# Optimization experiments

Measured on AMD Instinct MI355X. Metric: run time of the kernel, lower is better.

Reference implementation:

```python
import jax, jax.numpy as jnp
import numpy as np

VOCAB, EMBED = 100000, 128
B, QLEN, DLEN = 1024, 32, 256
KERNEL_NUM, SIGMA, EXACT_SIGMA = 11, 0.1, 0.001
EPS = 1e-8  # torch F.cosine_similarity eps


def _kernel_mus(n):
    l_mu = [1.0]
    if n == 1:
        return l_mu
    bin_size = 2.0 / (n - 1)
    l_mu.append(1 - bin_size / 2)
    for i in range(1, n - 1):
        l_mu.append(round(l_mu[i] - bin_size, 5))
    return list(reversed(l_mu))


def _kernel_sigmas(n, sigma, exact_sigma):
    l_sigma = [exact_sigma]
    if n == 1:
        return l_sigma
    l_sigma += [sigma] * (n - 1)
    return list(reversed(l_sigma))


MUS = jnp.asarray(np.array(_kernel_mus(KERNEL_NUM), dtype=np.float32))      # [K]
SIGMAS = jnp.asarray(np.array(_kernel_sigmas(KERNEL_NUM, SIGMA, EXACT_SIGMA), dtype=np.float32))  # [K]


def setup_inputs() -> dict:
    key = jax.random.key(0)
    k = jax.random.split(key, 7)
    return {
        "emb": jax.random.normal(k[0], (VOCAB, EMBED), dtype=jnp.float32),
        "mlp_w": jax.random.normal(k[1], (1, KERNEL_NUM), dtype=jnp.float32) * 0.3,
        "mlp_b": jax.random.normal(k[2], (1,), dtype=jnp.float32) * 0.1,
        "query1": jax.random.randint(k[3], (B, QLEN), 0, VOCAB, dtype=jnp.int32).astype(jnp.int64),
        "doc1": jax.random.randint(k[4], (B, DLEN), 0, VOCAB, dtype=jnp.int32).astype(jnp.int64),
        "query2": jax.random.randint(k[5], (B, QLEN), 0, VOCAB, dtype=jnp.int32).astype(jnp.int64),
        "doc2": jax.random.randint(k[6], (B, DLEN), 0, VOCAB, dtype=jnp.int32).astype(jnp.int64),
    }


def _predict(emb, mlp_w, mlp_b, query, doc):
    qe = emb[query]                               # [B,Q,E]
    de = emb[doc]                                 # [B,D,E]
    qn = jnp.linalg.norm(qe, axis=-1)             # [B,Q]
    dn = jnp.linalg.norm(de, axis=-1)             # [B,D]
    dots = jnp.einsum("bqe,bde->bqd", qe, de)    # [B,Q,D]
    sim = dots / jnp.maximum(qn[:, :, None] * dn[:, None, :], EPS)
    # multi-Gaussian soft histogram: exp(-(sim-mu)^2/(2 sigma^2)), sum over doc,
    # log1p, sum over query  -> [B,K]
    z = (sim[..., None] - MUS) / SIGMAS           # [B,Q,D,K]
    K = jnp.exp(-0.5 * z * z)
    pooled = jnp.log1p(K.sum(axis=2)).sum(axis=1)  # [B,K]
    return pooled @ mlp_w.T + mlp_b               # [B,1]


def reference(emb, mlp_w, mlp_b, query1, doc1, query2, doc2):
    logits_1 = _predict(emb, mlp_w, mlp_b, query1, doc1)
    logits_2 = _predict(emb, mlp_w, mlp_b, query2, doc2)
    return jax.nn.sigmoid(logits_1 - logits_2)    # [B,1]
```

## Files before the change

kernel.cpp:

```cpp
#include <hip/hip_runtime.h>
#include <math.h>
#include <stdint.h>

#define VOCAB 100000
#define NB    1024
#define QLEN  32
#define DLEN  256
#define EMBED 128
#define KNUM  11

typedef __attribute__((ext_vector_type(8))) short bf16x8;
typedef __attribute__((ext_vector_type(4))) float f32x4;

#define HALF_L2E 0.7213475204444817f
#define TWO_L2E  2.8853900817779268f
#define EM4      0.018315638888734179f

#define SSTR  68
#define SHALF (16 * SSTR)

__device__ __forceinline__ float ex2(float x)
{
    float r;
    asm("v_exp_f32 %0, %1" : "=v"(r) : "v"(x));
    return r;
}

__global__ __launch_bounds__(256)
void cvt_table(const float* __restrict__ emb, ushort* __restrict__ ebf,
               float* __restrict__ inorm)
{
    const int row = blockIdx.x * 8 + (threadIdx.x >> 5);
    const int l32 = threadIdx.x & 31;
    const float4 v = *((const float4*)(emb + (size_t)row * EMBED) + l32);
    union { float f; unsigned u; } x0, x1, x2, x3;
    x0.f = v.x; x1.f = v.y; x2.f = v.z; x3.f = v.w;
    const unsigned r0 = x0.u + 0x8000u, r1 = x1.u + 0x8000u;
    const unsigned r2 = x2.u + 0x8000u, r3 = x3.u + 0x8000u;
    uint2 packed;
    packed.x = (r0 >> 16) | (r1 & 0xFFFF0000u);
    packed.y = (r2 >> 16) | (r3 & 0xFFFF0000u);
    *((uint2*)(ebf + (size_t)row * EMBED) + l32) = packed;
    x0.u = r0 & 0xFFFF0000u; x1.u = r1 & 0xFFFF0000u;
    x2.u = r2 & 0xFFFF0000u; x3.u = r3 & 0xFFFF0000u;
    float n = x0.f * x0.f + x1.f * x1.f + x2.f * x2.f + x3.f * x3.f;
    #pragma unroll
    for (int m = 1; m < 32; m <<= 1) n += __shfl_xor(n, m);
    if (l32 == 0) inorm[row] = __builtin_amdgcn_rsqf(n);
}

__device__ __forceinline__ bf16x8 cvt8(const float* p, float& nacc)
{
    uint4 a = *((const uint4*)p);
    uint4 b = *((const uint4*)(p + 4));
    unsigned u[8] = {a.x, a.y, a.z, a.w, b.x, b.y, b.z, b.w};
    bf16x8 r;
    #pragma unroll
    for (int i = 0; i < 8; ++i) {
        const unsigned q = u[i] + 0x8000u;
        r[i] = (short)(q >> 16);
        union { unsigned uu; float ff; } g; g.uu = q & 0xFFFF0000u;
        nacc = fmaf(g.ff, g.ff, nacc);
    }
    return r;
}

__device__ __forceinline__ void pool_half(float* __restrict__ wtile,
                                          const f32x4* __restrict__ a,
                                          const float* __restrict__ riq,
                                          const float* __restrict__ idn,
                                          float (*__restrict__ stot)[12],
                                          int mtbase, int l15, int quad)
{
    #pragma unroll
    for (int nt = 0; nt < 4; ++nt)
        #pragma unroll
        for (int r = 0; r < 4; ++r)
            wtile[(quad * 4 + r) * SSTR + nt * 16 + l15] = a[nt][r] * riq[r] * idn[nt];

    const float* rp = wtile + l15 * SSTR + quad * 16;
    float ksum[KNUM];
    #pragma unroll
    for (int k = 0; k < KNUM; ++k) ksum[k] = 0.f;

    #pragma unroll
    for (int i = 0; i < 4; ++i) {
        const f32x4 sv = *((const f32x4*)(rp + 4 * i));
        #pragma unroll
        for (int e = 0; e < 4; ++e) {
            const float s  = sv[e];
            const float z  = fmaf(s, 10.f, -1.f);
            const float e0 = ex2(-HALF_L2E * (z * z));
            float ru = ex2(fmaf(z,  TWO_L2E, -TWO_L2E));
            float rd = ex2(fmaf(z, -TWO_L2E, -TWO_L2E));
            ksum[5] += e0;
            float tt = e0;
            tt *= ru; ksum[6] += tt; ru *= EM4;
            tt *= ru; ksum[7] += tt; ru *= EM4;
            tt *= ru; ksum[8] += tt; ru *= EM4;
            tt *= ru; ksum[9] += tt;
            tt = e0;
            tt *= rd; ksum[4] += tt; rd *= EM4;
            tt *= rd; ksum[3] += tt; rd *= EM4;
            tt *= rd; ksum[2] += tt; rd *= EM4;
            tt *= rd; ksum[1] += tt; rd *= EM4;
            tt *= rd; ksum[0] += tt;
            ksum[10] += (s > 0.995f) ? 1.f : 0.f;
        }
    }
    #pragma unroll
    for (int k = 0; k < KNUM; ++k) {
        ksum[k] += __shfl_xor(ksum[k], 16);
        ksum[k] += __shfl_xor(ksum[k], 32);
    }
    if (quad == 0) {
        #pragma unroll
        for (int k = 0; k < KNUM; ++k)
            atomicAdd(&stot[mtbase + l15][k], ksum[k]);
    }
}

__global__ __launch_bounds__(256, 3)
void knrm_pair4(const ushort* __restrict__ ebf,
                const float* __restrict__ inorm,
                const float* __restrict__ mlp_w,
                const int* __restrict__ q1, const int* __restrict__ d1,
                const int* __restrict__ q2, const int* __restrict__ d2,
                float* __restrict__ logits)
{
    const int b    = blockIdx.x;
    const int pair = blockIdx.y;
    const int t    = threadIdx.x;
    const int w    = t >> 6;
    const int l15  = t & 15;
    const int quad = (t & 63) >> 4;

    const int* __restrict__ qry = (pair == 0 ? q1 : q2) + b * QLEN;
    const int* __restrict__ doc = (pair == 0 ? d1 : d2) + b * DLEN;

    __shared__ __align__(16) float s_sim[4 * SHALF];
    __shared__ float s_tot[QLEN][12];

    const int qid0 = qry[l15], qid1 = qry[l15 + 16];
    int did[4];
    #pragma unroll
    for (int j = 0; j < 4; ++j) did[j] = doc[(w * 4 + j) * 16 + l15];

    bf16x8 a0[4], a1[4], bbf[4][4];
    {
        const ushort* qp0 = ebf + (size_t)qid0 * EMBED + quad * 8;
        const ushort* qp1 = ebf + (size_t)qid1 * EMBED + quad * 8;
        #pragma unroll
        for (int kk = 0; kk < 4; ++kk) {
            a0[kk] = *(const bf16x8*)(qp0 + kk * 32);
            a1[kk] = *(const bf16x8*)(qp1 + kk * 32);
        }
        #pragma unroll
        for (int j = 0; j < 4; ++j) {
            const ushort* dp = ebf + (size_t)did[j] * EMBED + quad * 8;
            #pragma unroll
            for (int kk = 0; kk < 4; ++kk)
                bbf[j][kk] = *(const bf16x8*)(dp + kk * 32);
        }
    }
    float idn[4];
    #pragma unroll
    for (int j = 0; j < 4; ++j) idn[j] = inorm[did[j]];
    float riq[2][4];
    #pragma unroll
    for (int r = 0; r < 4; ++r) {
        riq[0][r] = inorm[qry[quad * 4 + r]];
        riq[1][r] = inorm[qry[16 + quad * 4 + r]];
    }

    #pragma unroll
    for (int i = t; i < QLEN * 12; i += 256) ((float*)s_tot)[i] = 0.f;

    #pragma unroll
    for (int kk = 0; kk < 4; ++kk)
        asm volatile("" :: "v"(a0[kk]), "v"(a1[kk]));
    #pragma unroll
    for (int j = 0; j < 4; ++j)
        asm volatile("" :: "v"(bbf[j][0]), "v"(bbf[j][1]),
                          "v"(bbf[j][2]), "v"(bbf[j][3]));
    __builtin_amdgcn_sched_barrier(0);

    f32x4 acc[2][4];
    #pragma unroll
    for (int mt = 0; mt < 2; ++mt)
        #pragma unroll
        for (int j = 0; j < 4; ++j)
            acc[mt][j] = (f32x4){0.f, 0.f, 0.f, 0.f};
    #pragma unroll
    for (int kk = 0; kk < 4; ++kk)
        #pragma unroll
        for (int j = 0; j < 4; ++j) {
            acc[0][j] = __builtin_amdgcn_mfma_f32_16x16x32_bf16(a0[kk], bbf[j][kk], acc[0][j], 0, 0, 0);
            acc[1][j] = __builtin_amdgcn_mfma_f32_16x16x32_bf16(a1[kk], bbf[j][kk], acc[1][j], 0, 0, 0);
        }

    __syncthreads();

    float* wtile = s_sim + w * SHALF;
    pool_half(wtile, acc[0], riq[0], idn, s_tot, 0,  l15, quad);
    pool_half(wtile, acc[1], riq[1], idn, s_tot, 16, l15, quad);
    __syncthreads();

    if (t < QLEN) {
        float c = 0.f;
        #pragma unroll
        for (int k = 0; k < KNUM; ++k) c += mlp_w[k] * log1pf(s_tot[t][k]);
        #pragma unroll
        for (int mm = 1; mm < 32; mm <<= 1) c += __shfl_xor(c, mm);
        if (t == 0) logits[pair * NB + b] = c;
    }
}

template<bool PRE>
__global__ __launch_bounds__(256, 4)
void knrm_pair(const float* __restrict__ emb,
               const ushort* __restrict__ ebf,
               const float* __restrict__ inorm,
               const float* __restrict__ mlp_w,
               const int* __restrict__ q1, const int* __restrict__ d1,
               const int* __restrict__ q2, const int* __restrict__ d2,
               float* __restrict__ logits)
{
    const int b    = blockIdx.x;
    const int pair = blockIdx.y;
    const int t    = threadIdx.x;
    const int w    = t >> 6;
    const int l15  = t & 15;
    const int quad = (t & 63) >> 4;

    const int* __restrict__ qry = (pair == 0 ? q1 : q2) + b * QLEN;
    const int* __restrict__ doc = (pair == 0 ? d1 : d2) + b * DLEN;

    __shared__ __align__(16) float s_sim[4 * SHALF];
    __shared__ float s_tot[QLEN][12];

    #pragma unroll
    for (int i = t; i < QLEN * 12; i += 256) ((float*)s_tot)[i] = 0.f;
    __syncthreads();

    const int qid0 = qry[l15], qid1 = qry[l15 + 16];
    int did[4];
    #pragma unroll
    for (int nt = 0; nt < 4; ++nt) did[nt] = doc[(w * 4 + nt) * 16 + l15];

    f32x4 acc[2][4];
    #pragma unroll
    for (int mt = 0; mt < 2; ++mt)
        #pragma unroll
        for (int nt = 0; nt < 4; ++nt)
            acc[mt][nt] = (f32x4){0.f, 0.f, 0.f, 0.f};

    float idn[4], riq[2][4];
    float* wtile = s_sim + w * SHALF;

    if (PRE) {
        const ushort* qp0 = ebf + (size_t)qid0 * EMBED + quad * 8;
        const ushort* qp1 = ebf + (size_t)qid1 * EMBED + quad * 8;
        #pragma unroll
        for (int kk = 0; kk < 4; ++kk) {
            const bf16x8 a0 = *((const bf16x8*)(qp0 + kk * 32));
            const bf16x8 a1 = *((const bf16x8*)(qp1 + kk * 32));
            #pragma unroll
            for (int nt = 0; nt < 4; ++nt) {
                const bf16x8 bb = *((const bf16x8*)(ebf + (size_t)did[nt] * EMBED + quad * 8 + kk * 32));
                acc[0][nt] = __builtin_amdgcn_mfma_f32_16x16x32_bf16(a0, bb, acc[0][nt], 0, 0, 0);
                acc[1][nt] = __builtin_amdgcn_mfma_f32_16x16x32_bf16(a1, bb, acc[1][nt], 0, 0, 0);
            }
        }
        #pragma unroll
        for (int nt = 0; nt < 4; ++nt) idn[nt] = inorm[did[nt]];
        #pragma unroll
        for (int r = 0; r < 4; ++r) {
            riq[0][r] = inorm[qry[quad * 4 + r]];
            riq[1][r] = inorm[qry[16 + quad * 4 + r]];
        }
    } else {
        float qn2[2] = {0.f, 0.f}, dn2[4] = {0.f, 0.f, 0.f, 0.f};
        const float* qp0 = emb + (size_t)qid0 * EMBED + quad * 8;
        const float* qp1 = emb + (size_t)qid1 * EMBED + quad * 8;
        #pragma unroll
        for (int kk = 0; kk < 4; ++kk) {
            const bf16x8 a0 = cvt8(qp0 + kk * 32, qn2[0]);
            const bf16x8 a1 = cvt8(qp1 + kk * 32, qn2[1]);
            #pragma unroll
            for (int nt = 0; nt < 4; ++nt) {
                const bf16x8 bb = cvt8(emb + (size_t)did[nt] * EMBED + quad * 8 + kk * 32, dn2[nt]);
                acc[0][nt] = __builtin_amdgcn_mfma_f32_16x16x32_bf16(a0, bb, acc[0][nt], 0, 0, 0);
                acc[1][nt] = __builtin_amdgcn_mfma_f32_16x16x32_bf16(a1, bb, acc[1][nt], 0, 0, 0);
            }
        }
        #pragma unroll
        for (int i = 0; i < 2; ++i) {
            qn2[i] += __shfl_xor(qn2[i], 16);
            qn2[i] += __shfl_xor(qn2[i], 32);
        }
        #pragma unroll
        for (int nt = 0; nt < 4; ++nt) {
            dn2[nt] += __shfl_xor(dn2[nt], 16);
            dn2[nt] += __shfl_xor(dn2[nt], 32);
            idn[nt] = __builtin_amdgcn_rsqf(dn2[nt]);
        }
        #pragma unroll
        for (int r = 0; r < 4; ++r) {
            riq[0][r] = __builtin_amdgcn_rsqf(__shfl(qn2[0], quad * 4 + r));
            riq[1][r] = __builtin_amdgcn_rsqf(__shfl(qn2[1], quad * 4 + r));
        }
    }

    pool_half(wtile, acc[0], riq[0], idn, s_tot, 0,  l15, quad);
    pool_half(wtile, acc[1], riq[1], idn, s_tot, 16, l15, quad);
    __syncthreads();

    if (t < QLEN) {
        float c = 0.f;
        #pragma unroll
        for (int k = 0; k < KNUM; ++k) c += mlp_w[k] * log1pf(s_tot[t][k]);
        #pragma unroll
        for (int mm = 1; mm < 32; mm <<= 1) c += __shfl_xor(c, mm);
        if (t == 0) logits[pair * NB + b] = c;
    }
}

__global__ __launch_bounds__(256)
void knrm_combine(const float* __restrict__ logits, float* __restrict__ out)
{
    const int i = blockIdx.x * blockDim.x + threadIdx.x;
    if (i < NB) {
        const float d = logits[i] - logits[NB + i];
        out[i] = 1.f / (1.f + __expf(-d));
    }
}

extern "C" void kernel_launch(void* const* d_in, const int* in_sizes, int n_in,
                              void* d_out, int out_size, void* d_ws, size_t ws_size,
                              hipStream_t stream)
{
    const float* emb   = (const float*)d_in[0];
    const float* mlp_w = (const float*)d_in[1];
    const int* q1 = (const int*)d_in[3];
    const int* d1 = (const int*)d_in[4];
    const int* q2 = (const int*)d_in[5];
    const int* d2 = (const int*)d_in[6];

    float* out = (float*)d_out;

    const size_t need = 2 * NB * 4
                      + (size_t)VOCAB * 4
                      + (size_t)VOCAB * EMBED * 2 + 256;
    if (ws_size >= need) {
        float*  logits = (float*)d_ws;
        float*  inorm  = logits + 2 * NB;
        ushort* ebf    = (ushort*)(inorm + VOCAB);
        cvt_table<<<VOCAB / 8, 256, 0, stream>>>(emb, ebf, inorm);
        knrm_pair4<<<dim3(NB, 2), 256, 0, stream>>>(ebf, inorm, mlp_w,
                                                    q1, d1, q2, d2, logits);
    } else {
        float* logits = (float*)d_ws;
        knrm_pair<false><<<dim3(NB, 2), 256, 0, stream>>>(emb, nullptr, nullptr, mlp_w,
                                                          q1, d1, q2, d2, logits);
    }
    knrm_combine<<<(NB + 255) / 256, 256, 0, stream>>>((float*)d_ws, out);
}
```

Measured before the change: 137.9 us.

## Process both query/doc pairs per block, prefetching pair B during pair A pooling

Each block now handles both pairs for one batch row. Pair B's embedding gathers are issued before pair A's pooling so their latency overlaps with the pooling arithmetic, and the sigmoid combine is folded into the kernel, which drops the separate combine launch. The price is more live registers under a 3-wave occupancy bound and half as many blocks, which could cause spills or lower parallelism. The dead PRE path of the fallback kernel is also removed.

New measurement: 150.9 us. 9.4% more time.

```diff
diff --git a/kernel.cpp b/kernel.cpp
--- a/kernel.cpp
+++ b/kernel.cpp
@@ -121,35 +121,36 @@
 }
 
 __global__ __launch_bounds__(256, 3)
-void knrm_pair4(const ushort* __restrict__ ebf,
-                const float* __restrict__ inorm,
-                const float* __restrict__ mlp_w,
-                const int* __restrict__ q1, const int* __restrict__ d1,
-                const int* __restrict__ q2, const int* __restrict__ d2,
-                float* __restrict__ logits)
+void knrm_pair12(const ushort* __restrict__ ebf,
+                 const float* __restrict__ inorm,
+                 const float* __restrict__ mlp_w,
+                 const int* __restrict__ q1, const int* __restrict__ d1,
+                 const int* __restrict__ q2, const int* __restrict__ d2,
+                 float* __restrict__ out)
 {
     const int b    = blockIdx.x;
-    const int pair = blockIdx.y;
     const int t    = threadIdx.x;
     const int w    = t >> 6;
     const int l15  = t & 15;
     const int quad = (t & 63) >> 4;
 
-    const int* __restrict__ qry = (pair == 0 ? q1 : q2) + b * QLEN;
-    const int* __restrict__ doc = (pair == 0 ? d1 : d2) + b * DLEN;
+    const int* __restrict__ qryA = q1 + b * QLEN;
+    const int* __restrict__ docA = d1 + b * DLEN;
+    const int* __restrict__ qryB = q2 + b * QLEN;
+    const int* __restrict__ docB = d2 + b * DLEN;
 
     __shared__ __align__(16) float s_sim[4 * SHALF];
-    __shared__ float s_tot[QLEN][12];
-
-    const int qid0 = qry[l15], qid1 = qry[l15 + 16];
-    int did[4];
-    #pragma unroll
-    for (int j = 0; j < 4; ++j) did[j] = doc[(w * 4 + j) * 16 + l15];
+    __shared__ float s_tot[2][QLEN][12];
+
+    const int qidA0 = qryA[l15], qidA1 = qryA[l15 + 16];
+    int didA[4];
+    #pragma unroll
+    for (int j = 0; j < 4; ++j) didA[j] = docA[(w * 4 + j) * 16 + l15];
 
     bf16x8 a0[4], a1[4], bbf[4][4];
     {
-        const ushort* qp0 = ebf + (size_t)qid0 * EMBED + quad * 8;
-        const ushort* qp1 = ebf + (size_t)qid1 * EMBED + quad * 8;
+        const ushort* qp0 = ebf + (size_t)qidA0 * EMBED + quad * 8;
+        const ushort* qp1 = ebf + (size_t)qidA1 * EMBED + quad * 8;
         #pragma unroll
         for (int kk = 0; kk < 4; ++kk) {
             a0[kk] = *(const bf16x8*)(qp0 + kk * 32);
@@ -157,24 +158,24 @@
         }
         #pragma unroll
         for (int j = 0; j < 4; ++j) {
-            const ushort* dp = ebf + (size_t)did[j] * EMBED + quad * 8;
+            const ushort* dp = ebf + (size_t)didA[j] * EMBED + quad * 8;
             #pragma unroll
             for (int kk = 0; kk < 4; ++kk)
                 bbf[j][kk] = *(const bf16x8*)(dp + kk * 32);
         }
     }
-    float idn[4];
-    #pragma unroll
-    for (int j = 0; j < 4; ++j) idn[j] = inorm[did[j]];
-    float riq[2][4];
+    float idnA[4];
+    #pragma unroll
+    for (int j = 0; j < 4; ++j) idnA[j] = inorm[didA[j]];
+    float riqA[2][4];
     #pragma unroll
     for (int r = 0; r < 4; ++r) {
-        riq[0][r] = inorm[qry[quad * 4 + r]];
-        riq[1][r] = inorm[qry[16 + quad * 4 + r]];
-    }
-
-    #pragma unroll
-    for (int i = t; i < QLEN * 12; i += 256) ((float*)s_tot)[i] = 0.f;
+        riqA[0][r] = inorm[qryA[quad * 4 + r]];
+        riqA[1][r] = inorm[qryA[16 + quad * 4 + r]];
+    }
+
+    #pragma unroll
+    for (int i = t; i < 2 * QLEN * 12; i += 256) ((float*)s_tot)[i] = 0.f;
 
     #pragma unroll
     for (int kk = 0; kk < 4; ++kk)
@@ -185,34 +186,93 @@
                           "v"(bbf[j][2]), "v"(bbf[j][3]));
     __builtin_amdgcn_sched_barrier(0);
 
-    f32x4 acc[2][4];
+    f32x4 accA[2][4];
     #pragma unroll
     for (int mt = 0; mt < 2; ++mt)
         #pragma unroll
         for (int j = 0; j < 4; ++j)
-            acc[mt][j] = (f32x4){0.f, 0.f, 0.f, 0.f};
+            accA[mt][j] = (f32x4){0.f, 0.f, 0.f, 0.f};
     #pragma unroll
     for (int kk = 0; kk < 4; ++kk)
         #pragma unroll
         for (int j = 0; j < 4; ++j) {
-            acc[0][j] = __builtin_amdgcn_mfma_f32_16x16x32_bf16(a0[kk], bbf[j][kk], acc[0][j], 0, 0, 0);
-            acc[1][j] = __builtin_amdgcn_mfma_f32_16x16x32_bf16(a1[kk], bbf[j][kk], acc[1][j], 0, 0, 0);
+            accA[0][j] = __builtin_amdgcn_mfma_f32_16x16x32_bf16(a0[kk], bbf[j][kk], accA[0][j], 0, 0, 0);
+            accA[1][j] = __builtin_amdgcn_mfma_f32_16x16x32_bf16(a1[kk], bbf[j][kk], accA[1][j], 0, 0, 0);
         }
 
     __syncthreads();
 
+    const int qidB0 = qryB[l15], qidB1 = qryB[l15 + 16];
+    int didB[4];
+    #pragma unroll
+    for (int j = 0; j < 4; ++j) didB[j] = docB[(w * 4 + j) * 16 + l15];
+    bf16x8 aB0[4], aB1[4], bbfB[4][4];
+    {
+        const ushort* qp0 = ebf + (size_t)qidB0 * EMBED + quad * 8;
+        const ushort* qp1 = ebf + (size_t)qidB1 * EMBED + quad * 8;
+        #pragma unroll
+        for (int kk = 0; kk < 4; ++kk) {
+            aB0[kk] = *(const bf16x8*)(qp0 + kk * 32);
+            aB1[kk] = *(const bf16x8*)(qp1 + kk * 32);
+        }
+        #pragma unroll
+        for (int j = 0; j < 4; ++j) {
+            const ushort* dp = ebf + (size_t)didB[j] * EMBED + quad * 8;
+            #pragma unroll
+            for (int kk = 0; kk < 4; ++kk)
+                bbfB[j][kk] = *(const bf16x8*)(dp + kk * 32);
+        }
+    }
+    float idnB[4];
+    #pragma unroll
+    for (int j = 0; j < 4; ++j) idnB[j] = inorm[didB[j]];
+    float riqB[2][4];
+    #pragma unroll
+    for (int r = 0; r < 4; ++r) {
+        riqB[0][r] = inorm[qryB[quad * 4 + r]];
+        riqB[1][r] = inorm[qryB[16 + quad * 4 + r]];
+    }
+    __builtin_amdgcn_sched_barrier(0);
+
     float* wtile = s_sim + w * SHALF;
-    pool_half(wtile, acc[0], riq[0], idn, s_tot, 0,  l15, quad);
-    pool_half(wtile, acc[1], riq[1], idn, s_tot, 16, l15, quad);
+    pool_half(wtile, accA[0], riqA[0], idnA, s_tot[0], 0,  l15, quad);
+    pool_half(wtile, accA[1], riqA[1], idnA, s_tot[0], 16, l15, quad);
+
+    #pragma unroll
+    for (int kk = 0; kk < 4; ++kk)
+        asm volatile("" :: "v"(aB0[kk]), "v"(aB1[kk]));
+    #pragma unroll
+    for (int j = 0; j < 4; ++j)
+        asm volatile("" :: "v"(bbfB[j][0]), "v"(bbfB[j][1]),
+                          "v"(bbfB[j][2]), "v"(bbfB[j][3]));
+    __builtin_amdgcn_sched_barrier(0);
+
+    f32x4 accB[2][4];
+    #pragma unroll
+    for (int mt = 0; mt < 2; ++mt)
+        #pragma unroll
+        for (int j = 0; j < 4; ++j)
+            accB[mt][j] = (f32x4){0.f, 0.f, 0.f, 0.f};
+    #pragma unroll
+    for (int kk = 0; kk < 4; ++kk)
+        #pragma unroll
+        for (int j = 0; j < 4; ++j) {
+            accB[0][j] = __builtin_amdgcn_mfma_f32_16x16x32_bf16(aB0[kk], bbfB[j][kk], accB[0][j], 0, 0, 0);
+            accB[1][j] = __builtin_amdgcn_mfma_f32_16x16x32_bf16(aB1[kk], bbfB[j][kk], accB[1][j], 0, 0, 0);
+        }
+
+    pool_half(wtile, accB[0], riqB[0], idnB, s_tot[1], 0,  l15, quad);
+    pool_half(wtile, accB[1], riqB[1], idnB, s_tot[1], 16, l15, quad);
     __syncthreads();
 
     if (t < QLEN) {
         float c = 0.f;
         #pragma unroll
-        for (int k = 0; k < KNUM; ++k) c += mlp_w[k] * log1pf(s_tot[t][k]);
+        for (int k = 0; k < KNUM; ++k)
+            c += mlp_w[k] * (log1pf(s_tot[0][t][k]) - log1pf(s_tot[1][t][k]));
         #pragma unroll
         for (int mm = 1; mm < 32; mm <<= 1) c += __shfl_xor(c, mm);
-        if (t == 0) logits[pair * NB + b] = c;
+        if (t == 0) out[b] = 1.f / (1.f + __expf(-c));
     }
 }
 
@@ -258,28 +318,7 @@
     float idn[4], riq[2][4];
     float* wtile = s_sim + w * SHALF;
 
-    if (PRE) {
-        const ushort* qp0 = ebf + (size_t)qid0 * EMBED + quad * 8;
-        const ushort* qp1 = ebf + (size_t)qid1 * EMBED + quad * 8;
-        #pragma unroll
-        for (int kk = 0; kk < 4; ++kk) {
-            const bf16x8 a0 = *((const bf16x8*)(qp0 + kk * 32));
-            const bf16x8 a1 = *((const bf16x8*)(qp1 + kk * 32));
-            #pragma unroll
-            for (int nt = 0; nt < 4; ++nt) {
-                const bf16x8 bb = *((const bf16x8*)(ebf + (size_t)did[nt] * EMBED + quad * 8 + kk * 32));
-                acc[0][nt] = __builtin_amdgcn_mfma_f32_16x16x32_bf16(a0, bb, acc[0][nt], 0, 0, 0);
-                acc[1][nt] = __builtin_amdgcn_mfma_f32_16x16x32_bf16(a1, bb, acc[1][nt], 0, 0, 0);
-            }
-        }
-        #pragma unroll
-        for (int nt = 0; nt < 4; ++nt) idn[nt] = inorm[did[nt]];
-        #pragma unroll
-        for (int r = 0; r < 4; ++r) {
-            riq[0][r] = inorm[qry[quad * 4 + r]];
-            riq[1][r] = inorm[qry[16 + quad * 4 + r]];
-        }
-    } else {
+    {
         float qn2[2] = {0.f, 0.f}, dn2[4] = {0.f, 0.f, 0.f, 0.f};
         const float* qp0 = emb + (size_t)qid0 * EMBED + quad * 8;
         const float* qp1 = emb + (size_t)qid1 * EMBED + quad * 8;
@@ -353,16 +392,16 @@
                       + (size_t)VOCAB * 4
                       + (size_t)VOCAB * EMBED * 2 + 256;
     if (ws_size >= need) {
-        float*  logits = (float*)d_ws;
-        float*  inorm  = logits + 2 * NB;
-        ushort* ebf    = (ushort*)(inorm + VOCAB);
+        float*  scratch = (float*)d_ws;
+        float*  inorm   = scratch + 2 * NB;
+        ushort* ebf     = (ushort*)(inorm + VOCAB);
         cvt_table<<<VOCAB / 8, 256, 0, stream>>>(emb, ebf, inorm);
-        knrm_pair4<<<dim3(NB, 2), 256, 0, stream>>>(ebf, inorm, mlp_w,
-                                                    q1, d1, q2, d2, logits);
+        knrm_pair12<<<dim3(NB), 256, 0, stream>>>(ebf, inorm, mlp_w,
+                                                  q1, d1, q2, d2, out);
     } else {
         float* logits = (float*)d_ws;
         knrm_pair<false><<<dim3(NB, 2), 256, 0, stream>>>(emb, nullptr, nullptr, mlp_w,
                                                           q1, d1, q2, d2, logits);
-    }
-    knrm_combine<<<(NB + 255) / 256, 256, 0, stream>>>((float*)d_ws, out);
-}
+        knrm_combine<<<(NB + 255) / 256, 256, 0, stream>>>(logits, out);
+    }
+}
```
